# Performance work log

Hardware: AMD Instinct MI355X
Metric: run time of the kernel (lower is better)

## Reference

```python
import jax, jax.numpy as jnp
import numpy as np

CHAN = 24
INNER = 64
GROUPS = 8
M = 5
LAM = 1e-4
MAX_ITER = 25
BETA = 1.0
EPS = 1e-5
B, HH, WW = 128, 32, 32


def conv2d(x, w, b=None):
    # NCHW, OIHW, 3x3 SAME conv (padding = kernel//2)
    y = jax.lax.conv_general_dilated(x, w, (1, 1), 'SAME',
                                     dimension_numbers=('NCHW', 'OIHW', 'NCHW'))
    if b is not None:
        y = y + b[None, :, None, None]
    return y


def group_norm(x, g, b):
    bsz, c, h, w = x.shape
    xg = x.reshape(bsz, GROUPS, c // GROUPS, h, w)
    mu = xg.mean(axis=(2, 3, 4), keepdims=True)
    var = xg.var(axis=(2, 3, 4), keepdims=True)
    xn = ((xg - mu) / jnp.sqrt(var + EPS)).reshape(bsz, c, h, w)
    return xn * g[None, :, None, None] + b[None, :, None, None]


def batch_norm(x, g, b):
    # training-mode batch statistics over (N, H, W)
    mu = x.mean(axis=(0, 2, 3), keepdims=True)
    var = x.var(axis=(0, 2, 3), keepdims=True)
    return (x - mu) / jnp.sqrt(var + EPS) * g[None, :, None, None] + b[None, :, None, None]


def resnet_f(p, z, x):
    c1w, g1g, g1b, c2w, g2g, g2b, g3g, g3b = p
    y = group_norm(jax.nn.relu(conv2d(z, c1w)), g1g, g1b)
    return group_norm(jax.nn.relu(z + group_norm(x + conv2d(y, c2w), g2g, g2b)), g3g, g3b)


def anderson(f, x0):
    # Anderson acceleration, fixed MAX_ITER iterations (no host-sync tol break).
    bsz = x0.shape[0]
    d = x0.size // bsz
    X = jnp.zeros((bsz, M, d), x0.dtype)
    Fm = jnp.zeros((bsz, M, d), x0.dtype)
    f0 = f(x0).reshape(bsz, -1)
    X = X.at[:, 0].set(x0.reshape(bsz, -1))
    Fm = Fm.at[:, 0].set(f0)
    X = X.at[:, 1].set(f0)
    Fm = Fm.at[:, 1].set(f(f0.reshape(x0.shape)).reshape(bsz, -1))
    for k in range(2, MAX_ITER):
        n = min(k, M)
        G = Fm[:, :n] - X[:, :n]                       # [b, n, d]
        Hm = jnp.zeros((bsz, n + 1, n + 1), x0.dtype)
        Hm = Hm.at[:, 0, 1:].set(1.0).at[:, 1:, 0].set(1.0)
        Hm = Hm.at[:, 1:, 1:].set(jnp.einsum('bnd,bmd->bnm', G, G)
                                  + LAM * jnp.eye(n, dtype=x0.dtype)[None])
        yv = jnp.zeros((bsz, n + 1, 1), x0.dtype).at[:, 0, 0].set(1.0)
        alpha = jnp.linalg.solve(Hm, yv)[:, 1:, 0]     # [b, n]
        xnew = (BETA * jnp.einsum('bn,bnd->bd', alpha, Fm[:, :n])
                + (1.0 - BETA) * jnp.einsum('bn,bnd->bd', alpha, X[:, :n]))
        X = X.at[:, k % M].set(xnew)
        Fm = Fm.at[:, k % M].set(f(xnew.reshape(x0.shape)).reshape(bsz, -1))
    return X[:, (MAX_ITER - 1) % M].reshape(x0.shape)


def setup_inputs() -> dict:
    key = jax.random.key(0)
    ks = jax.random.split(key, 8)
    inp = {
        'x': jax.random.normal(ks[0], (B, 3, HH, WW), jnp.float32),
        'pre_conv_w': jax.random.normal(ks[1], (CHAN, 3, 3, 3), jnp.float32) * 0.1,
        'pre_conv_b': jnp.zeros((CHAN,), jnp.float32),
        'pre_bn_g': jnp.ones((CHAN,), jnp.float32),
        'pre_bn_b': jnp.zeros((CHAN,), jnp.float32),
        'f_conv1_w': jax.random.normal(ks[2], (INNER, CHAN, 3, 3), jnp.float32) * 0.01,
        'gn1_g': jnp.ones((INNER,), jnp.float32),
        'gn1_b': jnp.zeros((INNER,), jnp.float32),
        'f_conv2_w': jax.random.normal(ks[3], (CHAN, INNER, 3, 3), jnp.float32) * 0.01,
        'gn2_g': jnp.ones((CHAN,), jnp.float32),
        'gn2_b': jnp.zeros((CHAN,), jnp.float32),
        'gn3_g': jnp.ones((CHAN,), jnp.float32),
        'gn3_b': jnp.zeros((CHAN,), jnp.float32),
        'post_bn_g': jnp.ones((CHAN,), jnp.float32),
        'post_bn_b': jnp.zeros((CHAN,), jnp.float32),
        'fc_w': jax.random.normal(ks[4], (10, CHAN * 4 * 4), jnp.float32) * 0.05,
        'fc_b': jnp.zeros((10,), jnp.float32),
    }
    return inp


def reference(x, pre_conv_w, pre_conv_b, pre_bn_g, pre_bn_b,
              f_conv1_w, gn1_g, gn1_b, f_conv2_w, gn2_g, gn2_b, gn3_g, gn3_b,
              post_bn_g, post_bn_b, fc_w, fc_b):
    # pre: conv + BatchNorm
    xp = batch_norm(conv2d(x, pre_conv_w, pre_conv_b), pre_bn_g, pre_bn_b)
    p = (f_conv1_w, gn1_g, gn1_b, f_conv2_w, gn2_g, gn2_b, gn3_g, gn3_b)
    # DEQ fixed-point solve (eval path: train=False returns the fixed point)
    z_star = anderson(lambda z: resnet_f(p, z, xp), jnp.zeros_like(xp))
    z = resnet_f(p, z_star, xp)
    # post: relu -> BN -> avgpool(8,8) -> flatten -> linear
    h = batch_norm(jax.nn.relu(z), post_bn_g, post_bn_b)
    bsz, c, hh, ww = h.shape
    pooled = h.reshape(bsz, c, hh // 8, 8, ww // 8, 8).mean(axis=(3, 5))  # [B,C,4,4]
    return pooled.reshape(bsz, -1) @ fc_w.T + fc_b
```

## Files before the change

### kernel.cpp

```cpp
#include <hip/hip_runtime.h>
#include <hip/hip_bf16.h>

typedef __hip_bfloat16 bf16;
typedef unsigned short ushortT;
typedef __attribute__((ext_vector_type(8))) short short8;
typedef __attribute__((ext_vector_type(4))) float f32x4;

#define BB 128
#define CHAN 24
#define INNER 64
#define HW 1024
#define DD (CHAN*HW)

constexpr size_t cBD = (size_t)BB*DD;
constexpr size_t cYB = (size_t)BB*INNER*HW;

__device__ __attribute__((aligned(16))) ushortT g_xp[cBD];
__device__ __attribute__((aligned(16))) ushortT g_X[5*cBD];
__device__ __attribute__((aligned(16))) ushortT g_F[5*cBD];
__device__ __attribute__((aligned(16))) ushortT g_G[5*cBD];
__device__ __attribute__((aligned(16))) ushortT g_yb[cYB];
__device__ __attribute__((aligned(16))) ushortT g_tb[cBD];
__device__ __attribute__((aligned(16))) ushortT g_w1m[9*64*32];
__device__ __attribute__((aligned(16))) ushortT g_w2m[9*24*64];
__device__ __attribute__((aligned(16))) float g_stats2a[48];
__device__ __attribute__((aligned(16))) float g_stats2b[48];
__device__ __attribute__((aligned(16))) float g_gn1sum[BB*8*2];
__device__ __attribute__((aligned(16))) float g_gram[BB*25];
__device__ __attribute__((aligned(16))) float g_params[5120];
__device__ unsigned g_isbf16;

#define P_PCW 0
#define P_PCB 648
#define P_PBG 672
#define P_PBB 696
#define P_G1G 720
#define P_G1B 784
#define P_G2G 848
#define P_G2B 872
#define P_G3G 896
#define P_G3B 920
#define P_POG 944
#define P_POB 968
#define P_FCW 992
#define P_FCB 4832

__device__ __forceinline__ size_t aidx(int b, int icv, int pix){
  return (((size_t)b*3 + icv)*1024 + (size_t)pix)*8;
}
__device__ __forceinline__ float rdin(const void* p, int i){
  if (g_isbf16) return __bfloat162float(((const bf16*)p)[i]);
  return ((const float*)p)[i];
}
__device__ __forceinline__ float b2f(ushortT u){
  unsigned v = ((unsigned)u) << 16;
  return __builtin_bit_cast(float, v);
}
__device__ __forceinline__ ushortT f2b(float f){
  unsigned u = __builtin_bit_cast(unsigned, f);
  u += 0x7FFFu + ((u >> 16) & 1u);
  return (ushortT)(u >> 16);
}
__device__ __forceinline__ void ld24c(const ushortT* base, int b, int pix, float* o){
  #pragma unroll
  for (int icv=0;icv<3;icv++){
    short8 v = *(const short8*)&base[aidx(b,icv,pix)];
    #pragma unroll
    for (int j=0;j<8;j++) o[icv*8+j] = b2f((ushortT)v[j]);
  }
}
__device__ __forceinline__ void st24c(ushortT* base, int b, int pix, const float* i){
  #pragma unroll
  for (int icv=0;icv<3;icv++){
    short8 v;
    #pragma unroll
    for (int j=0;j<8;j++) v[j] = (short)f2b(i[icv*8+j]);
    *(short8*)&base[aidx(b,icv,pix)] = v;
  }
}

__global__ void detect_k(const void* g1g){
  if (threadIdx.x==0 && blockIdx.x==0){
    unsigned u = *(const unsigned*)g1g;
    g_isbf16 = (u == 0x3F803F80u) ? 1u : 0u;
  }
}

__global__ void cvt_params_k(const void* pcw, const void* pcb, const void* pbg, const void* pbb,
                             const void* g1g, const void* g1b, const void* g2g, const void* g2b,
                             const void* g3g, const void* g3b, const void* pog, const void* pob,
                             const void* fcw, const void* fcb){
  int t = threadIdx.x;
  for (int i=t;i<648;i+=256)  g_params[P_PCW+i]=rdin(pcw,i);
  for (int i=t;i<24;i+=256) { g_params[P_PCB+i]=rdin(pcb,i);
                              g_params[P_PBG+i]=rdin(pbg,i);
                              g_params[P_PBB+i]=rdin(pbb,i);
                              g_params[P_G2G+i]=rdin(g2g,i);
                              g_params[P_G2B+i]=rdin(g2b,i);
                              g_params[P_G3G+i]=rdin(g3g,i);
                              g_params[P_G3B+i]=rdin(g3b,i);
                              g_params[P_POG+i]=rdin(pog,i);
                              g_params[P_POB+i]=rdin(pob,i); }
  for (int i=t;i<64;i+=256) { g_params[P_G1G+i]=rdin(g1g,i);
                              g_params[P_G1B+i]=rdin(g1b,i); }
  for (int i=t;i<3840;i+=256) g_params[P_FCW+i]=rdin(fcw,i);
  for (int i=t;i<10;i+=256)   g_params[P_FCB+i]=rdin(fcb,i);
  for (int i=t;i<48;i+=256) { g_stats2a[i]=0.f; g_stats2b[i]=0.f; }
}

__global__ void wtm_k(const void* w1, const void* w2){
  int t = blockIdx.x*256 + threadIdx.x;
  if (t < 9*64*32){
    int ic = t & 31, oc = (t>>5)&63, s9 = t>>11;
    float v = (ic<24) ? rdin(w1, (oc*24+ic)*9 + s9) : 0.f;
    g_w1m[t] = f2b(v);
  }
  int u = t - 9*64*32;
  if (u >= 0 && u < 9*24*64){
    int ic = u & 63; int rest = u >> 6; int oc = rest % 24; int s9 = rest / 24;
    g_w2m[u] = f2b(rdin(w2, (oc*64+ic)*9 + s9));
  }
}

__global__ void zero0_k(){
  size_t base = ((size_t)blockIdx.x*256 + threadIdx.x)*8;
  short8 z = {0,0,0,0,0,0,0,0};
  *(short8*)&g_yb[base] = z;
  if (blockIdx.x < 1536) *(short8*)&g_X[base] = z;
  int t = blockIdx.x*256 + threadIdx.x;
  if (blockIdx.x < 8)  g_gn1sum[t] = 0.f;
}

__global__ void preconv_k(const void* __restrict__ x){
  __shared__ float sR2d[4*48];
  int id = blockIdx.x*256 + threadIdx.x;
  int b = id >> 10, pix = id & 1023;
  int yy = pix >> 5, xx = pix & 31;
  float acc[24];
  #pragma unroll
  for (int oc=0;oc<24;oc++) acc[oc] = g_params[P_PCB+oc];
  for (int ic=0; ic<3; ic++)
    for (int ky=0; ky<3; ky++){
      int gy = yy+ky-1; if (gy<0||gy>=32) continue;
      for (int kx=0;kx<3;kx++){
        int gx = xx+kx-1; if (gx<0||gx>=32) continue;
        float v = rdin(x, ((b*3+ic)*32+gy)*32+gx);
        #pragma unroll
        for (int oc=0;oc<24;oc++)
          acc[oc] += v * g_params[P_PCW+(oc*3+ic)*9+ky*3+kx];
      }
    }
  st24c(g_tb, b, pix, acc);
  int lane = threadIdx.x & 63, wv = threadIdx.x >> 6;
  #pragma unroll
  for (int c=0;c<24;c++){
    float r = acc[c], q = acc[c]*acc[c];
    #pragma unroll
    for (int off=32;off;off>>=1){ r += __shfl_down(r,off,64); q += __shfl_down(q,off,64); }
    if (lane==0){ sR2d[wv*48+c*2]=r; sR2d[wv*48+c*2+1]=q; }
  }
  __syncthreads();
  if (threadIdx.x < 48)
    atomicAdd(&g_stats2a[threadIdx.x],
      sR2d[threadIdx.x] + sR2d[48+threadIdx.x] + sR2d[96+threadIdx.x] + sR2d[144+threadIdx.x]);
}

__global__ void bn_apply_k(){
  int id = blockIdx.x*256+threadIdx.x;
  int b = id >> 10, pix = id & 1023;
  const float inv = 1.f/(BB*HW);
  float tv[24], ov[24];
  ld24c(g_tb, b, pix, tv);
  #pragma unroll
  for (int c=0;c<24;c++){
    float mean = g_stats2a[c*2]*inv;
    float var = fmaxf(g_stats2a[c*2+1]*inv - mean*mean, 0.f);
    float rstd = rsqrtf(var + 1e-5f);
    ov[c] = (tv[c]-mean)*rstd*g_params[P_PBG+c] + g_params[P_PBB+c];
  }
  st24c(g_xp, b, pix, ov);
}

__launch_bounds__(256, 2)
__global__ void conv1_k(int s){
  __shared__ ushortT sMem[29312];
  ushortT* sA = sMem;
  ushortT* sW = sMem + 10880;
  const int tid = threadIdx.x;
  const int lane = tid & 63, wv = tid >> 6;
  const int mLane = lane & 15, q = lane >> 4;
  const int bid = blockIdx.x;
  const int b = (bid & 7) + ((bid >> 5) << 3);
  const int yt = (bid >> 3) & 3;
  const ushortT* __restrict__ Xs = g_X + (size_t)s*cBD;
  for (int i = tid; i < 1360; i += 256){
    int icv = i & 3, apix = i >> 2;
    int yl = apix / 34, xl = apix - yl*34;
    int gy = yt*8 - 1 + yl, gx = xl - 1;
    short8 v = {0,0,0,0,0,0,0,0};
    if (gy >= 0 && gy < 32 && gx >= 0 && gx < 32 && icv < 3)
      v = *(const short8*)&Xs[aidx(b, icv, gy*32 + gx)];
    *(short8*)&sA[(size_t)(apix*4 + (icv ^ (apix&3)))*8] = v;
  }
  for (int i = tid; i < 2304; i += 256){
    int icv = i & 3, rest = i >> 2;
    int oc = rest & 63, s9 = rest >> 6;
    short8 v = *(const short8*)&g_w1m[(size_t)((s9*64 + oc)*32) + icv*8];
    *(short8*)&sW[(size_t)((s9*64+oc)*4 + (icv ^ (oc&3)))*8] = v;
  }
  __syncthreads();
  f32x4 acc[4][4];
  #pragma unroll
  for (int mt=0;mt<4;mt++)
    #pragma unroll
    for (int nt=0;nt<4;nt++) acc[mt][nt] = (f32x4){0.f,0.f,0.f,0.f};
  for (int s9=0; s9<9; s9++){
    int ky = s9/3, kx = s9 - ky*3;
    short8 bfr[4];
    #pragma unroll
    for (int nt=0;nt<4;nt++){
      int oc = nt*16 + mLane;
      bfr[nt] = *(const short8*)&sW[(size_t)((s9*64+oc)*4 + (q ^ (oc&3)))*8];
    }
    #pragma unroll
    for (int mt=0;mt<4;mt++){
      int g = wv*4+mt;
      int apix = ((g>>1) + ky)*34 + (g&1)*16 + mLane + kx;
      short8 afr = *(const short8*)&sA[(size_t)(apix*4 + (q ^ (apix&3)))*8];
      #pragma unroll
      for (int nt=0;nt<4;nt++)
        acc[mt][nt] = __builtin_amdgcn_mfma_f32_16x16x32_bf16(afr, bfr[nt], acc[mt][nt], 0,0,0);
    }
  }
  __syncthreads();
  ushortT* sOut = sMem;
  #pragma unroll
  for (int mt=0;mt<4;mt++){
    int g = wv*4+mt;
    #pragma unroll
    for (int nt=0;nt<4;nt++){
      int oc = nt*16 + mLane;
      #pragma unroll
      for (int r=0;r<4;r++){
        int pix = (g>>1)*32 + (g&1)*16 + q*4 + r;
        sOut[pix*64 + oc] = f2b(fmaxf(acc[mt][nt][r], 0.f));
      }
    }
  }
  __syncthreads();
  float s0=0.f, s1=0.f;
  size_t gbase = ((size_t)b*1024 + yt*256)*64;
  for (int c = tid; c < 2048; c += 256){
    short8 v = *(const short8*)&sOut[c*8];
    *(short8*)&g_yb[gbase + (size_t)c*8] = v;
    #pragma unroll
    for (int j=0;j<8;j++){ float f = b2f((ushortT)v[j]); s0 += f; s1 += f*f; }
  }
  s0 += __shfl_down(s0,32); s1 += __shfl_down(s1,32);
  s0 += __shfl_down(s0,16); s1 += __shfl_down(s1,16);
  s0 += __shfl_down(s0, 8); s1 += __shfl_down(s1, 8);
  if (lane < 8){
    atomicAdd(&g_gn1sum[(b*8+lane)*2],   s0);
    atomicAdd(&g_gn1sum[(b*8+lane)*2+1], s1);
  }
}

template<int N>
__device__ __forceinline__ void chol_alpha(const float Kf[5][5], float* alpha){
  double K[N][N];
  #pragma unroll
  for (int i=0;i<N;i++)
    #pragma unroll
    for (int j=0;j<N;j++)
      K[i][j] = (double)Kf[i][j] + (i==j ? 1e-4 : 0.0);
  #pragma unroll
  for (int c=0;c<N;c++){
    double d = K[c][c];
    #pragma unroll
    for (int k2=0;k2<c;k2++) d -= K[c][k2]*K[c][k2];
    d = sqrt(fmax(d, 1e-300));
    K[c][c] = d;
    double inv = 1.0/d;
    #pragma unroll
    for (int r=c+1;r<N;r++){
      double v = K[r][c];
      #pragma unroll
      for (int k2=0;k2<c;k2++) v -= K[r][k2]*K[c][k2];
      K[r][c] = v*inv;
    }
  }
  double y[N];
  #pragma unroll
  for (int i=0;i<N;i++){
    double v = 1.0;
    #pragma unroll
    for (int j=0;j<i;j++) v -= K[i][j]*y[j];
    y[i] = v / K[i][i];
  }
  double w[N];
  #pragma unroll
  for (int i=N-1;i>=0;i--){
    double v = y[i];
    #pragma unroll
    for (int j=i+1;j<N;j++) v -= K[j][i]*w[j];
    w[i] = v / K[i][i];
  }
  double sum = 0.0;
  #pragma unroll
  for (int i=0;i<N;i++) sum += w[i];
  double invs = 1.0/sum;
  #pragma unroll
  for (int i=0;i<N;i++) alpha[i] = (float)(w[i]*invs);
}

#define C2F_SMEM 161440

__launch_bounds__(1024)
__global__ void c2f_k(int s, int n, int snext){
  extern __shared__ __align__(16) ushortT sU[];
  ushortT* sYb = sU;
  ushortT* sTB = sU;
  ushortT* sW2 = sU + 65536;
  float* sS    = (float*)(sU + 79360);
  float* sAff1  = sS;
  float* sStat2 = sS + 128;
  float* sAff2  = sS + 176;
  float* sStat3 = sS + 224;
  float* sAff3  = sS + 240;
  float* sRed   = sS + 288;
  float* sRedG  = sS + 544;
  float* sAlpha = sS + 624;
  float* sFin   = (float*)sTB;

  const int b = blockIdx.x;
  const int t = threadIdx.x;
  const int lane = t & 63, wv = t >> 6;
  const int mLane = lane & 15, q = lane >> 4;
  const int g0 = wv*4;
  const bool ntOK = (mLane < 8);
  const bool fin = (n == 0);

  if (t < 64){
    const int c = t, gr = c>>3;
    float S = g_gn1sum[(b*8+gr)*2], Q = g_gn1sum[(b*8+gr)*2+1];
    float mean = S*(1.f/8192.f);
    float var  = fmaxf(Q*(1.f/8192.f) - mean*mean, 0.f);
    float rstd = rsqrtf(var + 1e-5f);
    float sc = rstd*g_params[P_G1G+c];
    sAff1[c] = sc; sAff1[64+c] = g_params[P_G1B+c] - mean*sc;
  }
  if (t < 16) g_gn1sum[b*16 + t] = 0.f;
  if (t >= 64 && t < 112) sStat2[t-64] = 0.f;
  if (t >= 112 && t < 128) sStat3[t-112] = 0.f;
  __syncthreads();

  for (int i=t; i<8192; i+=1024){
    int chk = i & 7, pix = i >> 3;
    short8 raw = *(const short8*)&g_yb[((size_t)b*1024 + pix)*64 + chk*8];
    short8 v;
    #pragma unroll
    for (int j=0;j<8;j++){
      int c = chk*8+j;
      v[j] = (short)f2b(b2f((ushortT)raw[j])*sAff1[c] + sAff1[64+c]);
    }
    *(short8*)&sYb[(size_t)(pix*8 + (chk^(pix&7)))*8] = v;
  }
  for (int i=t; i<1728; i+=1024){
    int icv=i&7, rest=i>>3, oc=rest%24, s9=rest/24;
    *(short8*)&sW2[(size_t)((s9*24+oc)*8 + (icv^(oc&7)))*8] =
      *(const short8*)&g_w2m[(size_t)((s9*24+oc)*64) + icv*8];
  }
  __syncthreads();

  f32x4 a2[4][2];
  #pragma unroll
  for (int mt=0;mt<4;mt++){ a2[mt][0]=(f32x4){0.f,0.f,0.f,0.f}; a2[mt][1]=(f32x4){0.f,0.f,0.f,0.f}; }
  for (int s9=0; s9<9; ++s9){
    const int ky = s9/3, kx = s9 - ky*3;
    #pragma unroll
    for (int ks=0; ks<2; ++ks){
      const int ch = ks*4 + q;
      short8 b0 = *(const short8*)&sW2[(size_t)((s9*24+mLane)*8 + (ch^(mLane&7)))*8];
      short8 b1 = ntOK ? *(const short8*)&sW2[(size_t)((s9*24+16+mLane)*8 + (ch^(mLane&7)))*8]
                       : (short8){0,0,0,0,0,0,0,0};
      #pragma unroll
      for (int mt=0;mt<4;mt++){
        const int g = g0+mt;
        const int gy = (g>>1) + ky - 1;
        const int gx = (g&1)*16 + mLane + kx - 1;
        short8 afr = {0,0,0,0,0,0,0,0};
        if (gy>=0 && gy<32 && gx>=0 && gx<32){
          const int pp = gy*32 + gx;
          afr = *(const short8*)&sYb[(size_t)(pp*8 + (ch^(pp&7)))*8];
        }
        a2[mt][0] = __builtin_amdgcn_mfma_f32_16x16x32_bf16(afr, b0, a2[mt][0], 0,0,0);
        a2[mt][1] = __builtin_amdgcn_mfma_f32_16x16x32_bf16(afr, b1, a2[mt][1], 0,0,0);
      }
    }
  }
  #pragma unroll
  for (int ci=0; ci<2; ++ci){
    const int oc = ci*16 + mLane;
    const bool ok = (ci==0) || ntOK;
    const int icv = oc>>3, e = oc&7;
    float s0=0.f, s1=0.f;
    if (ok){
      #pragma unroll
      for (int mt=0;mt<4;mt++){
        #pragma unroll
        for (int r=0;r<4;r++){
          const int pp = (g0+mt)*16 + q*4 + r;
          float v = a2[mt][ci][r] + b2f(g_xp[aidx(b,icv,pp)+e]);
          a2[mt][ci][r] = v;
          s0 += v; s1 += v*v;
        }
      }
    }
    s0 += __shfl_down(s0,32); s1 += __shfl_down(s1,32);
    s0 += __shfl_down(s0,16); s1 += __shfl_down(s1,16);
    if (lane < 16 && ok){
      atomicAdd(&sStat2[oc*2],   s0);
      atomicAdd(&sStat2[oc*2+1], s1);
    }
  }
  __syncthreads();

  #pragma unroll
  for (int ci=0; ci<2; ++ci){
    const int oc = ci*16 + mLane;
    if ((ci==0) || ntOK){
      const int icv = oc>>3, e = oc&7;
      #pragma unroll
      for (int mt=0;mt<4;mt++)
        #pragma unroll
        for (int r=0;r<4;r++){
          const int pp = (g0+mt)*16 + q*4 + r;
          sTB[(size_t)(pp*4 + (icv ^ ((pp>>2)&3)))*8 + e] = f2b(a2[mt][ci][r]);
        }
    }
  }
  if (t < 24){
    const int gr = t/3;
    float S = sStat2[(gr*3)*2]  +sStat2[(gr*3+1)*2]  +sStat2[(gr*3+2)*2];
    float Q = sStat2[(gr*3)*2+1]+sStat2[(gr*3+1)*2+1]+sStat2[(gr*3+2)*2+1];
    float m = S*(1.f/3072.f);
    float rstd = rsqrtf(fmaxf(Q*(1.f/3072.f)-m*m,0.f)+1e-5f);
    float sc = rstd*g_params[P_G2G+t];
    sAff2[t] = sc; sAff2[24+t] = g_params[P_G2B+t] - m*sc;
  }
  __syncthreads();

  float v[24], xv[24];
  #pragma unroll
  for (int i=0;i<3;i++){
    short8 t8 = *(const short8*)&sTB[(size_t)(t*4 + (i ^ ((t>>2)&3)))*8];
    #pragma unroll
    for (int j8=0;j8<8;j8++) v[i*8+j8] = b2f((ushortT)t8[j8]);
  }
  ld24c(g_X + (size_t)s*cBD, b, t, xv);
  float p0[8], p1[8];
  #pragma unroll
  for (int g=0;g<8;g++){ p0[g]=0.f; p1[g]=0.f; }
  #pragma unroll
  for (int c=0;c<24;c++){
    float val = fmaxf(xv[c] + v[c]*sAff2[c] + sAff2[24+c], 0.f);
    v[c] = val;
    int g = c/3;
    p0[g] += val; p1[g] += val*val;
  }
  #pragma unroll
  for (int g=0;g<8;g++){
    #pragma unroll
    for (int off=32;off;off>>=1){ p0[g]+=__shfl_down(p0[g],off,64); p1[g]+=__shfl_down(p1[g],off,64); }
  }
  if (lane==0){
    #pragma unroll
    for (int g=0;g<8;g++){ sRed[wv*16+g*2]=p0[g]; sRed[wv*16+g*2+1]=p1[g]; }
  }
  __syncthreads();
  if (t < 8){
    float S=0.f, Q=0.f;
    #pragma unroll
    for (int w=0;w<16;w++){ S += sRed[w*16+t*2]; Q += sRed[w*16+t*2+1]; }
    float m = S*(1.f/3072.f);
    sStat3[t*2]   = m;
    sStat3[t*2+1] = rsqrtf(fmaxf(Q*(1.f/3072.f) - m*m, 0.f) + 1e-5f);
  }
  __syncthreads();
  if (t < 24){
    int g = t/3;
    float sc = sStat3[g*2+1]*g_params[P_G3G+t];
    sAff3[t] = sc; sAff3[24+t] = g_params[P_G3B+t] - sStat3[g*2]*sc;
  }
  __syncthreads();
  float fv[24];
  #pragma unroll
  for (int c=0;c<24;c++) fv[c] = v[c]*sAff3[c] + sAff3[24+c];
  st24c(g_F + (size_t)s*cBD, b, t, fv);

  if (!fin){
    float gl[24];
    #pragma unroll
    for (int c=0;c<24;c++) gl[c] = b2f(f2b(fv[c] - xv[c]));
    st24c(g_G + (size_t)s*cBD, b, t, gl);
    float part[5];
    #pragma unroll
    for (int j=0;j<5;j++) part[j]=0.f;
    #pragma unroll
    for (int j=0;j<5;j++){
      if (j < n){
        float acc=0.f;
        if (j == s){
          #pragma unroll
          for (int c=0;c<24;c++) acc += gl[c]*gl[c];
        } else {
          float gv[24];
          ld24c(g_G + (size_t)j*cBD, b, t, gv);
          #pragma unroll
          for (int c=0;c<24;c++) acc += gl[c]*gv[c];
        }
        part[j] = acc;
      }
    }
    #pragma unroll
    for (int j=0;j<5;j++){
      float vv = part[j];
      #pragma unroll
      for (int off=32;off;off>>=1) vv += __shfl_down(vv,off,64);
      if (lane==0) sRedG[wv*5+j] = vv;
    }
    __syncthreads();
    if (t == 0){
      for (int j=0;j<n;j++){
        float vv = 0.f;
        for (int w=0;w<16;w++) vv += sRedG[w*5+j];
        g_gram[b*25+s*5+j] = vv;
        g_gram[b*25+j*5+s] = vv;
      }
      float Kf[5][5];
      for (int i=0;i<n;i++)
        for (int j=0;j<n;j++) Kf[i][j] = g_gram[b*25+i*5+j];
      float al[5];
      if (n==1) al[0]=1.f;
      else if (n==2) chol_alpha<2>(Kf, al);
      else if (n==3) chol_alpha<3>(Kf, al);
      else if (n==4) chol_alpha<4>(Kf, al);
      else chol_alpha<5>(Kf, al);
      for (int j=0;j<n;j++) sAlpha[j] = al[j];
    }
    __syncthreads();
    float al[5];
    #pragma unroll
    for (int j=0;j<5;j++) al[j] = (j<n) ? sAlpha[j] : 0.f;
    float xn[24];
    #pragma unroll
    for (int c=0;c<24;c++) xn[c] = 0.f;
    #pragma unroll
    for (int j=0;j<5;j++){
      if (j < n){
        if (j == s){
          #pragma unroll
          for (int c=0;c<24;c++) xn[c] += al[j]*b2f(f2b(fv[c]));
        } else {
          float fv2[24];
          ld24c(g_F + (size_t)j*cBD, b, t, fv2);
          #pragma unroll
          for (int c=0;c<24;c++) xn[c] += al[j]*fv2[c];
        }
      }
    }
    st24c(g_X + (size_t)snext*cBD, b, t, xn);
  } else {
    #pragma unroll
    for (int c=0;c<24;c++){
      float r = fmaxf(b2f(f2b(fv[c])), 0.f);
      float q2 = r*r;
      #pragma unroll
      for (int off=32;off;off>>=1){ r += __shfl_down(r,off,64); q2 += __shfl_down(q2,off,64); }
      if (lane==0){ sFin[wv*48+c*2]=r; sFin[wv*48+c*2+1]=q2; }
    }
    __syncthreads();
    if (t < 48){
      float vv = 0.f;
      #pragma unroll
      for (int w=0;w<16;w++) vv += sFin[w*48+t];
      atomicAdd(&g_stats2b[t], vv);
    }
  }
}

__global__ void postfc_k(void* __restrict__ out){
  __shared__ float sPool[384];
  __shared__ float sMean[24], sRstd[24];
  int b = blockIdx.x, t = threadIdx.x;
  if (t < 24){
    const float inv = 1.f/(BB*HW);
    float mean = g_stats2b[t*2]*inv;
    float var = fmaxf(g_stats2b[t*2+1]*inv - mean*mean, 0.f);
    sMean[t] = mean; sRstd[t] = rsqrtf(var + 1e-5f);
  }
  __syncthreads();
  const ushortT* z = g_F + 4*cBD;
  for (int i=t; i<384; i+=256){
    int c = i>>4, bin = i&15, ph = bin>>2, pw = bin&3;
    int icv = c>>3, e = c&7;
    float gg = g_params[P_POG+c], bv = g_params[P_POB+c];
    float mean = sMean[c], rstd = sRstd[c];
    float sum = 0.f;
    for (int dy=0;dy<8;dy++)
      for (int dx=0;dx<8;dx++){
        int pix = (ph*8+dy)*32 + pw*8+dx;
        float vv = fmaxf(b2f(z[aidx(b,icv,pix) + e]), 0.f);
        sum += (vv-mean)*rstd*gg + bv;
      }
    sPool[i] = sum*(1.f/64.f);
  }
  __syncthreads();
  if (t < 10){
    float s2 = g_params[P_FCB+t];
    for (int k2=0;k2<384;k2++) s2 += sPool[k2]*g_params[P_FCW+t*384+k2];
    if (g_isbf16) ((bf16*)out)[b*10+t] = __float2bfloat16(s2);
    else ((float*)out)[b*10+t] = s2;
  }
}

extern "C" void kernel_launch(void* const* d_in, const int* in_sizes, int n_in,
                              void* d_out, int out_size, void* d_ws, size_t ws_size,
                              hipStream_t stream){
  const void* x   = d_in[0];
  const void* pcw = d_in[1];
  const void* pcb = d_in[2];
  const void* pbg = d_in[3];
  const void* pbb = d_in[4];
  const void* w1  = d_in[5];
  const void* g1g = d_in[6];
  const void* g1b = d_in[7];
  const void* w2  = d_in[8];
  const void* g2g = d_in[9];
  const void* g2b = d_in[10];
  const void* g3g = d_in[11];
  const void* g3b = d_in[12];
  const void* pog = d_in[13];
  const void* pob = d_in[14];
  const void* fcw = d_in[15];
  const void* fcb = d_in[16];
  (void)d_ws; (void)ws_size; (void)in_sizes; (void)n_in; (void)out_size;

  static bool attrSet = false;
  if (!attrSet){
    hipFuncSetAttribute(reinterpret_cast<const void*>(c2f_k),
                        hipFuncAttributeMaxDynamicSharedMemorySize, C2F_SMEM);
    attrSet = true;
  }

  detect_k<<<1,64,0,stream>>>(g1g);
  cvt_params_k<<<1,256,0,stream>>>(pcw,pcb,pbg,pbb,g1g,g1b,g2g,g2b,g3g,g3b,pog,pob,fcw,fcb);
  wtm_k<<<126,256,0,stream>>>(w1, w2);

  preconv_k<<<512,256,0,stream>>>(x);
  bn_apply_k<<<512,256,0,stream>>>();

  zero0_k<<<4096,256,0,stream>>>();
  c2f_k<<<128,1024,C2F_SMEM,stream>>>(0, 1, 1);

  for (int k=1;k<25;k++){
    int s = k%5;
    conv1_k<<<512,256,0,stream>>>(s);
    if (k < 24){
      int n = (k+1 < 5) ? (k+1) : 5;
      c2f_k<<<128,1024,C2F_SMEM,stream>>>(s, n, (k+1)%5);
    } else {
      c2f_k<<<128,1024,C2F_SMEM,stream>>>(s, 0, 0);
    }
  }

  postfc_k<<<128,256,0,stream>>>(d_out);
}
```

Baseline: 1.372 ms.

## Store xp in tile-major layout and prefetch residual loads in c2f kernel

```diff
diff --git a/kernel.cpp b/kernel.cpp
--- a/kernel.cpp
+++ b/kernel.cpp
@@ -4,6 +4,7 @@
 typedef __hip_bfloat16 bf16;
 typedef unsigned short ushortT;
 typedef __attribute__((ext_vector_type(8))) short short8;
+typedef __attribute__((ext_vector_type(4))) short s16x4;
 typedef __attribute__((ext_vector_type(4))) float f32x4;
 
 #define BB 128
@@ -47,6 +48,9 @@
 
 __device__ __forceinline__ size_t aidx(int b, int icv, int pix){
   return (((size_t)b*3 + icv)*1024 + (size_t)pix)*8;
+}
+__device__ __forceinline__ size_t tidx(int b, int g, int c, int p){
+  return ((((size_t)b*64 + g)*24 + c)<<4) + p;
 }
 __device__ __forceinline__ float rdin(const void* p, int i){
   if (g_isbf16) return __bfloat162float(((const bf16*)p)[i]);
@@ -169,16 +173,17 @@
   int id = blockIdx.x*256+threadIdx.x;
   int b = id >> 10, pix = id & 1023;
   const float inv = 1.f/(BB*HW);
-  float tv[24], ov[24];
+  float tv[24];
   ld24c(g_tb, b, pix, tv);
+  int g = pix >> 4, p = pix & 15;
   #pragma unroll
   for (int c=0;c<24;c++){
     float mean = g_stats2a[c*2]*inv;
     float var = fmaxf(g_stats2a[c*2+1]*inv - mean*mean, 0.f);
     float rstd = rsqrtf(var + 1e-5f);
-    ov[c] = (tv[c]-mean)*rstd*g_params[P_PBG+c] + g_params[P_PBB+c];
-  }
-  st24c(g_xp, b, pix, ov);
+    float ov = (tv[c]-mean)*rstd*g_params[P_PBG+c] + g_params[P_PBB+c];
+    g_xp[tidx(b,g,c,p)] = f2b(ov);
+  }
 }
 
 __launch_bounds__(256, 2)
@@ -325,7 +330,6 @@
   float* sAff1  = sS;
   float* sStat2 = sS + 128;
   float* sAff2  = sS + 176;
-  float* sStat3 = sS + 224;
   float* sAff3  = sS + 240;
   float* sRed   = sS + 288;
   float* sRedG  = sS + 544;
@@ -351,7 +355,6 @@
   }
   if (t < 16) g_gn1sum[b*16 + t] = 0.f;
   if (t >= 64 && t < 112) sStat2[t-64] = 0.f;
-  if (t >= 112 && t < 128) sStat3[t-112] = 0.f;
   __syncthreads();
 
   for (int i=t; i<8192; i+=1024){
@@ -371,6 +374,18 @@
       *(const short8*)&g_w2m[(size_t)((s9*24+oc)*64) + icv*8];
   }
   __syncthreads();
+
+  s16x4 xpv[2][4];
+  #pragma unroll
+  for (int ci=0; ci<2; ++ci)
+    #pragma unroll
+    for (int mt=0; mt<4; ++mt){
+      const int oc = ci*16 + mLane;
+      if (ci==0 || ntOK)
+        xpv[ci][mt] = *(const s16x4*)&g_xp[tidx(b, g0+mt, oc, q*4)];
+      else
+        xpv[ci][mt] = (s16x4){0,0,0,0};
+    }
 
   f32x4 a2[4][2];
   #pragma unroll
@@ -402,15 +417,13 @@
   for (int ci=0; ci<2; ++ci){
     const int oc = ci*16 + mLane;
     const bool ok = (ci==0) || ntOK;
-    const int icv = oc>>3, e = oc&7;
     float s0=0.f, s1=0.f;
     if (ok){
       #pragma unroll
       for (int mt=0;mt<4;mt++){
         #pragma unroll
         for (int r=0;r<4;r++){
-          const int pp = (g0+mt)*16 + q*4 + r;
-          float v = a2[mt][ci][r] + b2f(g_xp[aidx(b,icv,pp)+e]);
+          float v = a2[mt][ci][r] + b2f((ushortT)xpv[ci][mt][r]);
           a2[mt][ci][r] = v;
           s0 += v; s1 += v*v;
         }
@@ -424,6 +437,11 @@
     }
   }
   __syncthreads();
+
+  short8 xv8[3];
+  #pragma unroll
+  for (int i=0;i<3;i++)
+    xv8[i] = *(const short8*)&g_X[(size_t)s*cBD + aidx(b,i,t)];
 
   #pragma unroll
   for (int ci=0; ci<2; ++ci){
@@ -455,9 +473,11 @@
   for (int i=0;i<3;i++){
     short8 t8 = *(const short8*)&sTB[(size_t)(t*4 + (i ^ ((t>>2)&3)))*8];
     #pragma unroll
-    for (int j8=0;j8<8;j8++) v[i*8+j8] = b2f((ushortT)t8[j8]);
-  }
-  ld24c(g_X + (size_t)s*cBD, b, t, xv);
+    for (int j8=0;j8<8;j8++){
+      v[i*8+j8]  = b2f((ushortT)t8[j8]);
+      xv[i*8+j8] = b2f((ushortT)xv8[i][j8]);
+    }
+  }
   float p0[8], p1[8];
   #pragma unroll
   for (int g=0;g<8;g++){ p0[g]=0.f; p1[g]=0.f; }
@@ -478,19 +498,15 @@
     for (int g=0;g<8;g++){ sRed[wv*16+g*2]=p0[g]; sRed[wv*16+g*2+1]=p1[g]; }
   }
   __syncthreads();
-  if (t < 8){
+  if (t < 24){
+    const int g = t/3;
     float S=0.f, Q=0.f;
     #pragma unroll
-    for (int w=0;w<16;w++){ S += sRed[w*16+t*2]; Q += sRed[w*16+t*2+1]; }
+    for (int w=0;w<16;w++){ S += sRed[w*16+g*2]; Q += sRed[w*16+g*2+1]; }
     float m = S*(1.f/3072.f);
-    sStat3[t*2]   = m;
-    sStat3[t*2+1] = rsqrtf(fmaxf(Q*(1.f/3072.f) - m*m, 0.f) + 1e-5f);
-  }
-  __syncthreads();
-  if (t < 24){
-    int g = t/3;
-    float sc = sStat3[g*2+1]*g_params[P_G3G+t];
-    sAff3[t] = sc; sAff3[24+t] = g_params[P_G3B+t] - sStat3[g*2]*sc;
+    float rstd = rsqrtf(fmaxf(Q*(1.f/3072.f) - m*m, 0.f) + 1e-5f);
+    float sc = rstd*g_params[P_G3G+t];
+    sAff3[t] = sc; sAff3[24+t] = g_params[P_G3B+t] - m*sc;
   }
   __syncthreads();
   float fv[24];
```

Measured after the change: 1.417 ms. 1.03x slower.
